# Kernel tuning notes

Hardware: AMD Instinct MI355X
Metric: run time of the kernel (lower is better)

## Reference

```python
import jax, jax.numpy as jnp
import numpy as np

B, T, C = 2, 2048, 2048
H, HD = 16, 128          # n_head, head_dim
LORA = C // 4            # kv_lora_rank = n_embd // compression_ratio
RD = HD // 2             # qk_rope_dim
ND = HD - RD             # qk_nope_dim
THETA = 100000.0


def setup_inputs() -> dict:
    key = jax.random.key(0)
    k0, k1, k2, k3, k4 = jax.random.split(key, 5)
    s = 0.02
    return {
        "x": jax.random.normal(k0, (B, T, C), dtype=jnp.float32),
        "Wq": jax.random.normal(k1, (C, H * HD), dtype=jnp.float32) * s,
        "Wkva": jax.random.normal(k2, (C, LORA + RD), dtype=jnp.float32) * s,
        "Wkvb": jax.random.normal(k3, (LORA, H * ND), dtype=jnp.float32) * s,
        "Wo": jax.random.normal(k4, (H * HD, C), dtype=jnp.float32) * s,
    }


def apply_rope(x, theta=THETA):
    # x: [B, H, T, D] with D even; interleaved complex rotation (torch.view_as_complex style)
    b, h, t, d = x.shape
    freqs = 1.0 / (theta ** (jnp.arange(0, d, 2, dtype=jnp.float32) / d))  # [D/2]
    ang = jnp.arange(t, dtype=jnp.float32)[:, None] * freqs[None, :]       # [T, D/2]
    cos, sin = jnp.cos(ang), jnp.sin(ang)
    xr = x.reshape(b, h, t, d // 2, 2)
    x0, x1 = xr[..., 0], xr[..., 1]
    o0 = x0 * cos - x1 * sin
    o1 = x0 * sin + x1 * cos
    return jnp.stack([o0, o1], axis=-1).reshape(b, h, t, d)


def reference(x, Wq, Wkva, Wkvb, Wo):
    Bx, Tx, Cx = x.shape
    # query projection -> [B, H, T, HD]
    q = (x @ Wq).reshape(Bx, Tx, H, HD).transpose(0, 2, 1, 3)
    # compressed KV + shared (MQA) rope key
    ckv = x @ Wkva                                  # [B, T, LORA+RD]
    kv_latent = ckv[..., :LORA]                     # [B, T, LORA]
    k_rope = ckv[..., LORA:]                        # [B, T, RD]
    # decompress nope part of K (== nope part of V)
    kv = (kv_latent @ Wkvb).reshape(Bx, Tx, H, ND).transpose(0, 2, 1, 3)  # [B,H,T,ND]
    k_rope = jnp.broadcast_to(k_rope[:, None, :, :], (Bx, H, Tx, RD))
    q_nope, q_rope = q[..., :ND], q[..., ND:]
    q_rope = apply_rope(q_rope)
    k_rope = apply_rope(k_rope)
    qf = jnp.concatenate([q_nope, q_rope], axis=-1)               # [B,H,T,HD]
    kf = jnp.concatenate([kv, k_rope], axis=-1)                   # [B,H,T,HD]
    vf = jnp.concatenate([kv, jnp.zeros_like(k_rope)], axis=-1)   # [B,H,T,HD]
    scale = 1.0 / np.sqrt(HD).astype(np.float32)
    att = jnp.einsum("bhtd,bhsd->bhts", qf, kf) * scale           # [B,H,T,T]
    causal = jnp.tril(jnp.ones((Tx, Tx), dtype=bool))
    att = jnp.where(causal, att, -jnp.inf)
    att = jax.nn.softmax(att, axis=-1)
    y = jnp.einsum("bhts,bhsd->bhtd", att, vf)                    # [B,H,T,HD]
    y = y.transpose(0, 2, 1, 3).reshape(Bx, Tx, H * HD)
    return y @ Wo
```

## Files before the change

### kernel.cpp

```cpp
#include <hip/hip_runtime.h>
#include <hip/hip_bf16.h>
#include <math.h>

#define B_ 2
#define T_ 2048
#define C_ 2048
#define H_ 16
#define HD_ 128
#define LORA_ 512
#define RD_ 64
#define ND_ 64
#define BT_ (B_*T_)
#define NKVA_ 576
#define NKVAP_ 640
#define LOG2_THETA 16.609640474436812f

typedef __bf16 bf16x8 __attribute__((ext_vector_type(8)));
typedef float  f32x4  __attribute__((ext_vector_type(4)));

#define MFMA16(a,b,c) __builtin_amdgcn_mfma_f32_16x16x32_bf16((a),(b),(c),0,0,0)

__device__ static inline void load_lds16(const __bf16* g, __bf16* l) {
  auto* lp = (__attribute__((address_space(3))) char*)(uintptr_t)(l);
  auto* gp = (const __attribute__((address_space(1))) char*)(g);
  __builtin_amdgcn_global_load_lds(gp, lp, 16, 0, 0);
}

__device__ static inline unsigned pkbf(float a, float b) {
  union { __bf16 h[2]; unsigned u; } v;
  v.h[0] = (__bf16)a; v.h[1] = (__bf16)b;
  return v.u;
}

__global__ __launch_bounds__(256) void k_cast_x(const float* __restrict__ x,
                                                __bf16* __restrict__ xb, int n) {
  int idx = blockIdx.x * 256 + threadIdx.x;
  if (idx < n) xb[idx] = (__bf16)x[idx];
}

__global__ __launch_bounds__(256) void k_tcast(const float* __restrict__ src,
                                               __bf16* __restrict__ dst,
                                               int K, int N, int NP) {
  __shared__ float tile[32][33];
  int k0 = blockIdx.x * 32;
  int n0 = blockIdx.y * 32;
  int tx = threadIdx.x & 31, ty = threadIdx.x >> 5;
  for (int i = ty; i < 32; i += 8) {
    int n = n0 + tx;
    tile[i][tx] = (n < N) ? src[(size_t)(k0 + i) * N + n] : 0.0f;
  }
  __syncthreads();
  for (int i = ty; i < 32; i += 8) {
    dst[(size_t)(n0 + i) * K + k0 + tx] = (__bf16)tile[tx][i];
  }
}

__global__ __launch_bounds__(256) void k_tcast_wo(const float* __restrict__ Wo,
                                                  __bf16* __restrict__ dst) {
  __shared__ float tile[32][33];
  int kc0 = blockIdx.x * 32;
  int n0  = blockIdx.y * 32;
  int rbase = (kc0 >> 6) * 128 + (kc0 & 63);
  int tx = threadIdx.x & 31, ty = threadIdx.x >> 5;
  for (int i = ty; i < 32; i += 8)
    tile[i][tx] = Wo[(size_t)(rbase + i) * C_ + n0 + tx];
  __syncthreads();
  for (int i = ty; i < 32; i += 8)
    dst[(size_t)(n0 + i) * 1024 + kc0 + tx] = (__bf16)tile[tx][i];
}

__global__ __launch_bounds__(256) void k_gemm_bt(const __bf16* __restrict__ A,
                                                 const __bf16* __restrict__ B,
                                                 float* __restrict__ C,
                                                 int M, int N, int K) {
  __shared__ __align__(16) __bf16 As[2][128 * 32];
  __shared__ __align__(16) __bf16 Bs[2][128 * 32];
  const int tid  = threadIdx.x;
  const int lane = tid & 63;
  const int wave = tid >> 6;
  const int bm = blockIdx.x, bn = blockIdx.y;
  const int r0 = tid >> 2;
  const int c8 = (tid & 3) * 8;
  const __bf16* Ag = A + (size_t)(bm * 128 + r0) * K + c8;
  const __bf16* Bg = B + (size_t)(bn * 128 + r0) * K + c8;
  const int wr = (wave >> 1) * 64, wc = (wave & 1) * 64;
  const int fr = lane & 15, fk = (lane >> 4) * 8;
  const f32x4 fzero = {0.f, 0.f, 0.f, 0.f};
  f32x4 acc[4][4];
#pragma unroll
  for (int i = 0; i < 4; ++i)
#pragma unroll
    for (int j = 0; j < 4; ++j) acc[i][j] = fzero;

  load_lds16(Ag,                  &As[0][tid * 8]);
  load_lds16(Ag + (size_t)64 * K, &As[0][tid * 8 + 2048]);
  load_lds16(Bg,                  &Bs[0][tid * 8]);
  load_lds16(Bg + (size_t)64 * K, &Bs[0][tid * 8 + 2048]);

  int buf = 0;
  for (int k0 = 0; k0 < K; k0 += 32) {
    __syncthreads();
    if (k0 + 32 < K) {
      const int nb = buf ^ 1;
      load_lds16(Ag + k0 + 32,                  &As[nb][tid * 8]);
      load_lds16(Ag + (size_t)64 * K + k0 + 32, &As[nb][tid * 8 + 2048]);
      load_lds16(Bg + k0 + 32,                  &Bs[nb][tid * 8]);
      load_lds16(Bg + (size_t)64 * K + k0 + 32, &Bs[nb][tid * 8 + 2048]);
    }
    bf16x8 af[4], bfg[4];
#pragma unroll
    for (int i = 0; i < 4; ++i) af[i]  = *(const bf16x8*)&As[buf][(wr + i * 16 + fr) * 32 + fk];
#pragma unroll
    for (int j = 0; j < 4; ++j) bfg[j] = *(const bf16x8*)&Bs[buf][(wc + j * 16 + fr) * 32 + fk];
#pragma unroll
    for (int i = 0; i < 4; ++i)
#pragma unroll
      for (int j = 0; j < 4; ++j)
        acc[i][j] = MFMA16(af[i], bfg[j], acc[i][j]);
    buf ^= 1;
  }
  const int rbase = (lane >> 4) * 4;
  float* Cb = C + (size_t)(bm * 128 + wr + rbase) * N + bn * 128 + wc + fr;
#pragma unroll
  for (int i = 0; i < 4; ++i)
#pragma unroll
    for (int j = 0; j < 4; ++j)
#pragma unroll
      for (int r = 0; r < 4; ++r)
        Cb[(size_t)(i * 16 + r) * N + j * 16] = acc[i][j][r];
}

__global__ __launch_bounds__(256) void k_rope_q(const float* __restrict__ q,
                                                __bf16* __restrict__ qf) {
  const float scale2 = 1.4426950408889634f / 11.313708498984760f;
  int idx = blockIdx.x * 256 + threadIdx.x;
  int d  = idx & 127;
  int t  = (idx >> 7) & 2047;
  int bh = idx >> 18;
  int h  = bh & 15, b = bh >> 4;
  const float* qrow = q + ((size_t)(b * T_ + t)) * 2048 + h * 128;
  float v;
  if (d < 64) {
    v = qrow[d];
  } else {
    int i = (d - 64) >> 1;
    float freq = exp2f(-((float)(2 * i) / 64.0f) * LOG2_THETA);
    float ang = (float)t * freq;
    float c = cosf(ang), s = sinf(ang);
    float x0 = qrow[64 + 2 * i], x1 = qrow[64 + 2 * i + 1];
    v = (d & 1) ? (x0 * s + x1 * c) : (x0 * c - x1 * s);
  }
  qf[idx] = (__bf16)(v * scale2);
}


__global__ __launch_bounds__(256) void k_rope_kf(const float* __restrict__ ckv,
                                                 __bf16* __restrict__ Kp) {
  int idx = blockIdx.x * 256 + threadIdx.x;
  int i = idx & 31;
  int t = (idx >> 5) & 2047;
  int h = (idx >> 16) & 15;
  int b = idx >> 20;
  const float* src = ckv + ((size_t)(b * T_ + t)) * NKVAP_ + 512;
  float freq = exp2f(-((float)(2 * i) / 64.0f) * LOG2_THETA);
  float ang = (float)t * freq;
  float c = cosf(ang), s = sinf(ang);
  float x0 = src[2 * i], x1 = src[2 * i + 1];
  float v0 = x0 * c - x1 * s;
  float v1 = x0 * s + x1 * c;
  int bh = b * 16 + h;
  int tile = t >> 6, cg = (t >> 4) & 3, frk = t & 15;
  int kg = 2 + (i >> 4), qd = (i >> 2) & 3, e = (2 * i) & 7;
  size_t off = (((size_t)(bh * 32 + tile) * 16) + cg * 4 + kg) * 512
             + (qd * 16 + frk) * 8 + e;
  *(unsigned*)(Kp + off) = pkbf(v0, v1);
}

__global__ __launch_bounds__(256) void k_cast_kvl(const float* __restrict__ ckv,
                                                  __bf16* __restrict__ kvl) {
  int idx = blockIdx.x * 256 + threadIdx.x;
  int r = idx >> 9, c = idx & 511;
  kvl[idx] = (__bf16)ckv[(size_t)r * NKVAP_ + c];
}

__global__ __launch_bounds__(256) void k_pack_kv(const float* __restrict__ kv,
                                                 __bf16* __restrict__ Kp,
                                                 __bf16* __restrict__ Vp) {
  __shared__ float tile[64][65];
  const int bh = blockIdx.x;
  const int b = bh >> 4, h = bh & 15;
  const int t0 = blockIdx.y * 64;
  const int tilei = t0 >> 6;
  const int tid = threadIdx.x;
  const int i0 = tid >> 4, d4 = (tid & 15) * 4;
  const int kg = d4 >> 5, qd = (d4 >> 3) & 3, e = d4 & 7;
#pragma unroll
  for (int p = 0; p < 4; ++p) {
    int i = i0 + p * 16;
    const float* src = kv + ((size_t)(b * T_ + t0 + i)) * 1024 + h * 64 + d4;
    float4 v = *(const float4*)src;
    tile[i][d4] = v.x; tile[i][d4 + 1] = v.y; tile[i][d4 + 2] = v.z; tile[i][d4 + 3] = v.w;
    union { __bf16 hh[4]; uint2 u; } o;
    o.hh[0] = (__bf16)v.x; o.hh[1] = (__bf16)v.y; o.hh[2] = (__bf16)v.z; o.hh[3] = (__bf16)v.w;
    const int cg = i >> 4, frk = i & 15;
    size_t koff = (((size_t)(bh * 32 + tilei) * 16) + cg * 4 + kg) * 512
                + (qd * 16 + frk) * 8 + e;
    *(uint2*)(Kp + koff) = o.u;
  }
  __syncthreads();
  const int dd = tid >> 2, tc0 = (tid & 3) * 16;
  __bf16 outv[16];
#pragma unroll
  for (int j = 0; j < 16; ++j) outv[j] = (__bf16)tile[tc0 + j][dd];
  const int g = dd >> 4, frv = dd & 15;
  const int ks = tc0 >> 5, qv = (tc0 >> 3) & 3;
  size_t voff = (((size_t)(bh * 32 + tilei) * 8) + g * 2 + ks) * 512
              + (qv * 16 + frv) * 8;
  *(bf16x8*)(Vp + voff) = *(bf16x8*)&outv[0];
  *(bf16x8*)(Vp + voff + 128) = *(bf16x8*)&outv[8];
}

__global__ __launch_bounds__(256, 3) void k_attn(const __bf16* __restrict__ qf,
                                                 const __bf16* __restrict__ Kp,
                                                 const __bf16* __restrict__ Vp,
                                                 __bf16* __restrict__ yc) {
  const int blk = blockIdx.x;
  const int bh = blk & 31;
  const int qt = 31 - (blk >> 5);
  const int b = bh >> 4, h = bh & 15;
  const int qbase = qt * 64;
  const int tid = threadIdx.x;
  const int lane = tid & 63, wave = tid >> 6;
  const int fr = lane & 15, quad = lane >> 4, fk8 = quad * 8;

  const int qi = qbase + wave * 16 + fr;
  const __bf16* qb = qf + ((size_t)bh * T_ + qi) * HD_;
  bf16x8 aq[4];
#pragma unroll
  for (int g = 0; g < 4; ++g) aq[g] = *(const bf16x8*)(qb + g * 32 + fk8);

  const f32x4 fzero = {0.f, 0.f, 0.f, 0.f};
  f32x4 accO[4];
#pragma unroll
  for (int g = 0; g < 4; ++g) accO[g] = fzero;
  float m = -1e30f, l = 0.f;

  const __bf16* kb = Kp + (size_t)bh * 32 * 8192 + (size_t)lane * 8;
  const __bf16* vb = Vp + (size_t)bh * 32 * 4096 + (size_t)lane * 8;
  const int srcA = (quad & 1) * 32 + fr, srcB = srcA + 16;
  const int hi = quad >> 1;

  for (int s0 = 0; s0 <= qbase; s0 += 64) {
    const __bf16* kt = kb + (size_t)(s0 >> 6) * 8192;
    const __bf16* vt = vb + (size_t)(s0 >> 6) * 4096;

    bf16x8 kr[4][4];
#pragma unroll
    for (int cg = 0; cg < 4; ++cg)
#pragma unroll
      for (int kg = 0; kg < 4; ++kg)
        kr[cg][kg] = *(const bf16x8*)(kt + (cg * 4 + kg) * 512);

    f32x4 accST[4];
#pragma unroll
    for (int cg = 0; cg < 4; ++cg) accST[cg] = fzero;
    __builtin_amdgcn_s_setprio(1);
#pragma unroll
    for (int cg = 0; cg < 4; ++cg) {
#pragma unroll
      for (int kg = 0; kg < 4; ++kg)
        accST[cg] = MFMA16(kr[cg][kg], aq[kg], accST[cg]);
    }
    __builtin_amdgcn_s_setprio(0);

    bf16x8 vr[4][2];
#pragma unroll
    for (int g = 0; g < 4; ++g)
#pragma unroll
      for (int ks = 0; ks < 2; ++ks)
        vr[g][ks] = *(const bf16x8*)(vt + (g * 2 + ks) * 512);

    float lmax = -1e30f;
    if (s0 == qbase) {
#pragma unroll
      for (int cg = 0; cg < 4; ++cg) {
#pragma unroll
        for (int r = 0; r < 4; ++r) {
          const int key = s0 + cg * 16 + quad * 4 + r;
          float v = accST[cg][r];
          v = (key <= qi) ? v : -1e30f;
          accST[cg][r] = v;
          lmax = fmaxf(lmax, v);
        }
      }
    } else {
#pragma unroll
      for (int cg = 0; cg < 4; ++cg) {
#pragma unroll
        for (int r = 0; r < 4; ++r) lmax = fmaxf(lmax, accST[cg][r]);
      }
    }
    lmax = fmaxf(lmax, __shfl_xor(lmax, 16, 64));
    lmax = fmaxf(lmax, __shfl_xor(lmax, 32, 64));

    if (!__all(lmax <= m + 8.0f)) {
      const float mn = fmaxf(m, lmax);
      const float alpha = exp2f(m - mn);
      l *= alpha;
#pragma unroll
      for (int g = 0; g < 4; ++g)
#pragma unroll
        for (int r = 0; r < 4; ++r) accO[g][r] *= alpha;
      m = mn;
    }

    float lsum = 0.f;
    unsigned pk0[4], pk1[4];
#pragma unroll
    for (int cg = 0; cg < 4; ++cg) {
      float p0 = exp2f(accST[cg][0] - m);
      float p1 = exp2f(accST[cg][1] - m);
      float p2 = exp2f(accST[cg][2] - m);
      float p3 = exp2f(accST[cg][3] - m);
      lsum += (p0 + p1) + (p2 + p3);
      pk0[cg] = pkbf(p0, p1);
      pk1[cg] = pkbf(p2, p3);
    }
    lsum += __shfl_xor(lsum, 16, 64);
    lsum += __shfl_xor(lsum, 32, 64);
    l += lsum;

#pragma unroll
    for (int ks = 0; ks < 2; ++ks) {
      int a0 = __shfl((int)pk0[2 * ks], srcA, 64);
      int b0 = __shfl((int)pk0[2 * ks + 1], srcA, 64);
      int a1 = __shfl((int)pk1[2 * ks], srcA, 64);
      int b1 = __shfl((int)pk1[2 * ks + 1], srcA, 64);
      int a2 = __shfl((int)pk0[2 * ks], srcB, 64);
      int b2 = __shfl((int)pk0[2 * ks + 1], srcB, 64);
      int a3 = __shfl((int)pk1[2 * ks], srcB, 64);
      int b3 = __shfl((int)pk1[2 * ks + 1], srcB, 64);
      union { int i[4]; bf16x8 v; } pf;
      pf.i[0] = hi ? b0 : a0;
      pf.i[1] = hi ? b1 : a1;
      pf.i[2] = hi ? b2 : a2;
      pf.i[3] = hi ? b3 : a3;
      __builtin_amdgcn_s_setprio(1);
#pragma unroll
      for (int g = 0; g < 4; ++g)
        accO[g] = MFMA16(vr[g][ks], pf.v, accO[g]);
      __builtin_amdgcn_s_setprio(0);
    }
  }

  const float linv = 1.0f / l;
  __bf16* yb = yc + ((size_t)(b * T_ + qi)) * 1024 + h * 64 + quad * 4;
#pragma unroll
  for (int g = 0; g < 4; ++g) {
    union { unsigned u[2]; uint2 v; } o;
    o.u[0] = pkbf(accO[g][0] * linv, accO[g][1] * linv);
    o.u[1] = pkbf(accO[g][2] * linv, accO[g][3] * linv);
    *(uint2*)(yb + g * 16) = o.v;
  }
}

extern "C" void kernel_launch(void* const* d_in, const int* in_sizes, int n_in,
                              void* d_out, int out_size, void* d_ws, size_t ws_size,
                              hipStream_t stream) {
  const float* x    = (const float*)d_in[0];
  const float* Wq   = (const float*)d_in[1];
  const float* Wkva = (const float*)d_in[2];
  const float* Wkvb = (const float*)d_in[3];
  const float* Wo   = (const float*)d_in[4];
  float* out = (float*)d_out;
  char* ws = (char*)d_ws;

  size_t off = 0;
  __bf16* xb    = (__bf16*)(ws + off); off += (size_t)BT_ * C_ * 2;
  __bf16* WqT   = (__bf16*)(ws + off); off += (size_t)2048 * 2048 * 2;
  __bf16* WkvaT = (__bf16*)(ws + off); off += (size_t)NKVAP_ * 2048 * 2;
  __bf16* WkvbT = (__bf16*)(ws + off); off += (size_t)1024 * 512 * 2;
  __bf16* WoTc  = (__bf16*)(ws + off); off += (size_t)2048 * 1024 * 2;
  float*  q     = (float*)(ws + off);  off += (size_t)BT_ * 2048 * 4;
  float*  ckv   = (float*)(ws + off);  off += (size_t)BT_ * NKVAP_ * 4;
  __bf16* kvl   = (__bf16*)(ws + off); off += (size_t)BT_ * 512 * 2;
  float*  kv    = (float*)(ws + off);  off += (size_t)BT_ * 1024 * 4;
  __bf16* qfb   = (__bf16*)(ws + off); off += (size_t)B_ * H_ * T_ * HD_ * 2;
  __bf16* yc    = (__bf16*)(ws + off); off += (size_t)BT_ * 1024 * 2;
  __bf16* Kp = (__bf16*)q;
  __bf16* Vp = (__bf16*)((char*)q + (size_t)B_ * H_ * T_ * HD_ * 2);

  k_cast_x<<<(BT_ * C_) / 256, 256, 0, stream>>>(x, xb, BT_ * C_);
  k_tcast<<<dim3(2048 / 32, 2048 / 32), 256, 0, stream>>>(Wq, WqT, 2048, 2048, 2048);
  k_tcast<<<dim3(2048 / 32, NKVAP_ / 32), 256, 0, stream>>>(Wkva, WkvaT, 2048, NKVA_, NKVAP_);
  k_tcast<<<dim3(512 / 32, 1024 / 32), 256, 0, stream>>>(Wkvb, WkvbT, 512, 1024, 1024);
  k_tcast_wo<<<dim3(1024 / 32, 2048 / 32), 256, 0, stream>>>(Wo, WoTc);

  k_gemm_bt<<<dim3(BT_ / 128, 2048 / 128), 256, 0, stream>>>(xb, WqT, q, BT_, 2048, 2048);
  k_gemm_bt<<<dim3(BT_ / 128, NKVAP_ / 128), 256, 0, stream>>>(xb, WkvaT, ckv, BT_, NKVAP_, 2048);

  k_rope_q<<<(B_ * H_ * T_ * HD_) / 256, 256, 0, stream>>>(q, qfb);
  k_cast_kvl<<<(BT_ * 512) / 256, 256, 0, stream>>>(ckv, kvl);

  k_gemm_bt<<<dim3(BT_ / 128, 1024 / 128), 256, 0, stream>>>(kvl, WkvbT, kv, BT_, 1024, 512);
  k_pack_kv<<<dim3(B_ * H_, T_ / 64), 256, 0, stream>>>(kv, Kp, Vp);
  k_rope_kf<<<(B_ * H_ * T_ * 32) / 256, 256, 0, stream>>>(ckv, Kp);

  k_attn<<<(T_ / 64) * B_ * H_, 256, 0, stream>>>(qfb, Kp, Vp, yc);

  k_gemm_bt<<<dim3(BT_ / 128, 2048 / 128), 256, 0, stream>>>(yc, WoTc, out, BT_, 2048, 1024);
}
```

Measured before the change: 343.4 us.

## Split attention KV loop across two wave groups and merge softmax partials in LDS

Doubles the attention block to 512 threads, so that two groups of four waves each handle alternating 64-key tiles for the same query rows. At the end, the odd group writes its partial output, running max and sum to shared memory, and the even group merges them with rescaling before writing the result. This aims to raise parallelism and latency hiding on the long causal rows. In exchange it adds LDS traffic, a block-wide barrier, and duplicate Q loads. The launch bound of 512 threads with 8 blocks may also constrain register allocation.

```diff
diff --git a/kernel.cpp b/kernel.cpp
--- a/kernel.cpp
+++ b/kernel.cpp
@@ -220,7 +220,7 @@
   *(bf16x8*)(Vp + voff + 128) = *(bf16x8*)&outv[8];
 }
 
-__global__ __launch_bounds__(256, 3) void k_attn(const __bf16* __restrict__ qf,
+__global__ __launch_bounds__(512, 8) void k_attn(const __bf16* __restrict__ qf,
                                                  const __bf16* __restrict__ Kp,
                                                  const __bf16* __restrict__ Vp,
                                                  __bf16* __restrict__ yc) {
@@ -231,9 +231,13 @@
   const int qbase = qt * 64;
   const int tid = threadIdx.x;
   const int lane = tid & 63, wave = tid >> 6;
+  const int w4 = wave & 3, par = wave >> 2;
   const int fr = lane & 15, quad = lane >> 4, fk8 = quad * 8;
 
-  const int qi = qbase + wave * 16 + fr;
+  __shared__ __align__(16) f32x4 mrgO[4][64][4];
+  __shared__ float mrgML[4][64][2];
+
+  const int qi = qbase + w4 * 16 + fr;
   const __bf16* qb = qf + ((size_t)bh * T_ + qi) * HD_;
   bf16x8 aq[4];
 #pragma unroll
@@ -250,7 +254,7 @@
   const int srcA = (quad & 1) * 32 + fr, srcB = srcA + 16;
   const int hi = quad >> 1;
 
-  for (int s0 = 0; s0 <= qbase; s0 += 64) {
+  for (int s0 = par * 64; s0 <= qbase; s0 += 128) {
     const __bf16* kt = kb + (size_t)(s0 >> 6) * 8192;
     const __bf16* vt = vb + (size_t)(s0 >> 6) * 4096;
 
@@ -353,14 +357,31 @@
     }
   }
 
-  const float linv = 1.0f / l;
-  __bf16* yb = yc + ((size_t)(b * T_ + qi)) * 1024 + h * 64 + quad * 4;
-#pragma unroll
-  for (int g = 0; g < 4; ++g) {
-    union { unsigned u[2]; uint2 v; } o;
-    o.u[0] = pkbf(accO[g][0] * linv, accO[g][1] * linv);
-    o.u[1] = pkbf(accO[g][2] * linv, accO[g][3] * linv);
-    *(uint2*)(yb + g * 16) = o.v;
+  if (par) {
+#pragma unroll
+    for (int g = 0; g < 4; ++g) mrgO[w4][lane][g] = accO[g];
+    mrgML[w4][lane][0] = m;
+    mrgML[w4][lane][1] = l;
+  }
+  __syncthreads();
+  if (!par) {
+    const float m1 = mrgML[w4][lane][0];
+    const float l1 = mrgML[w4][lane][1];
+    const float mn = fmaxf(m, m1);
+    const float a0 = exp2f(m - mn), a1 = exp2f(m1 - mn);
+    const float lt = l * a0 + l1 * a1;
+    const float linv = 1.0f / lt;
+    __bf16* yb = yc + ((size_t)(b * T_ + qi)) * 1024 + h * 64 + quad * 4;
+#pragma unroll
+    for (int g = 0; g < 4; ++g) {
+      f32x4 o1 = mrgO[w4][lane][g];
+      union { unsigned u[2]; uint2 v; } o;
+      o.u[0] = pkbf((accO[g][0] * a0 + o1[0] * a1) * linv,
+                    (accO[g][1] * a0 + o1[1] * a1) * linv);
+      o.u[1] = pkbf((accO[g][2] * a0 + o1[2] * a1) * linv,
+                    (accO[g][3] * a0 + o1[3] * a1) * linv);
+      *(uint2*)(yb + g * 16) = o.v;
+    }
   }
 }
 
@@ -406,7 +427,7 @@
   k_pack_kv<<<dim3(B_ * H_, T_ / 64), 256, 0, stream>>>(kv, Kp, Vp);
   k_rope_kf<<<(B_ * H_ * T_ * 32) / 256, 256, 0, stream>>>(ckv, Kp);
 
-  k_attn<<<(T_ / 64) * B_ * H_, 256, 0, stream>>>(qfb, Kp, Vp, yc);
+  k_attn<<<(T_ / 64) * B_ * H_, 512, 0, stream>>>(qfb, Kp, Vp, yc);
 
   k_gemm_bt<<<dim3(BT_ / 128, 2048 / 128), 256, 0, stream>>>(yc, WoTc, out, BT_, 2048, 1024);
 }
```

After: 810.6 us. 2.36x slower.
